# Optimization experiments

Hardware: AMD Instinct MI355X
Metric: run time of the kernel (lower is better)

The kernel has to match this reference:

```python
import jax, jax.numpy as jnp
import numpy as np

VERTS = [5023, 1256, 314, 79, 20]
SPIRAL_LEN = 9
T_FRAMES = 32
LATENT = 64


def _spiral_conv(x, idx, W, b):
    # x: [B, N, C]; idx: [N, L]; gather spiral neighborhoods then linear
    B = x.shape[0]
    g = x[:, idx.reshape(-1), :].reshape(B, idx.shape[0], -1)  # [B, N, L*C]
    return g @ W.T + b


def _pool(x, rows, cols, vals, n_out):
    # sparse matmul: out[b, rows] += x[b, cols] * vals  (index_select + scatter_add)
    gathered = x[:, cols, :] * vals[None, :, None]
    return jnp.zeros((x.shape[0], n_out, x.shape[2]), x.dtype).at[:, rows, :].add(gathered)


def _lstm_dir(x, Wih, Whh, bih, bhh, reverse):
    # x: [T, B, D]; PyTorch gate order i, f, g, o
    Bz, H = x.shape[1], Whh.shape[1]
    bias = bih + bhh
    def step(carry, xt):
        h, c = carry
        g = xt @ Wih.T + h @ Whh.T + bias
        i, f, gg, o = jnp.split(g, 4, axis=-1)
        c = jax.nn.sigmoid(f) * c + jax.nn.sigmoid(i) * jnp.tanh(gg)
        h = jax.nn.sigmoid(o) * jnp.tanh(c)
        return (h, c), h
    init = (jnp.zeros((Bz, H), x.dtype), jnp.zeros((Bz, H), x.dtype))
    _, hs = jax.lax.scan(step, init, x, reverse=reverse)
    return hs


def _forward(audio_hidden, vertices, actor,
             sp_idx0, sp_idx1, sp_idx2, sp_idx3,
             d0_rows, d0_cols, d0_vals, d1_rows, d1_cols, d1_vals,
             d2_rows, d2_cols, d2_vals, d3_rows, d3_cols, d3_vals,
             u0_rows, u0_cols, u0_vals, u1_rows, u1_cols, u1_vals,
             u2_rows, u2_cols, u2_vals, u3_rows, u3_cols, u3_vals,
             enc_W0, enc_b0, enc_W1, enc_b1, enc_W2, enc_b2, enc_W3, enc_b3,
             enc_lin_W, enc_lin_b, dec_lin_W, dec_lin_b,
             dec_W0, dec_b0, dec_W1, dec_b1, dec_W2, dec_b2, dec_W3, dec_b3,
             dec_W4, dec_b4, aud_W, aud_b,
             l0_Wih, l0_Whh, l0_bih, l0_bhh, l12_Wih, l12_Whh, l12_bih, l12_bhh):
    ah = audio_hidden
    if ah.shape[1] % 2 != 0:
        ah = ah[:, :ah.shape[1] - 1]
    tv = vertices.shape[1]
    if ah.shape[1] > 2 * tv:
        ah = ah[:, :2 * tv]
    elif ah.shape[1] < 2 * tv:
        tv = ah.shape[1] // 2
    hs = ah.reshape(1, ah.shape[1] // 2, ah.shape[2] * 2)[:, :tv]  # [1, T, 1536]
    audio_emb = hs @ aud_W.T + aud_b                                # [1, T, LATENT]
    # --- mesh encoder on actor template: (spiral conv -> ELU -> down pool) x4 -> Linear ---
    sp = (sp_idx0, sp_idx1, sp_idx2, sp_idx3)
    down = ((d0_rows, d0_cols, d0_vals), (d1_rows, d1_cols, d1_vals),
            (d2_rows, d2_cols, d2_vals), (d3_rows, d3_cols, d3_vals))
    encp = ((enc_W0, enc_b0), (enc_W1, enc_b1), (enc_W2, enc_b2), (enc_W3, enc_b3))
    x = actor
    for i in range(4):
        x = jax.nn.elu(_spiral_conv(x, sp[i], *encp[i]))
        x = _pool(x, *down[i], VERTS[i + 1])
    z = x.reshape(x.shape[0], -1) @ enc_lin_W.T + enc_lin_b        # [1, LATENT]
    actor_emb = jnp.broadcast_to(z[:, None, :], audio_emb.shape)
    # --- 3-layer bidirectional LSTM ---
    h = jnp.concatenate([audio_emb, actor_emb], axis=-1).transpose(1, 0, 2)  # [T, 1, 2*LATENT]
    for layer in range(3):
        if layer == 0:
            Wih, Whh, bih, bhh = l0_Wih, l0_Whh, l0_bih, l0_bhh
        else:
            Wih, Whh, bih, bhh = l12_Wih[layer - 1], l12_Whh[layer - 1], l12_bih[layer - 1], l12_bhh[layer - 1]
        f = _lstm_dir(h, Wih[0], Whh[0], bih[0], bhh[0], False)
        r = _lstm_dir(h, Wih[1], Whh[1], bih[1], bhh[1], True)
        h = jnp.concatenate([f, r], axis=-1)
    latent = h.transpose(1, 0, 2)[0]                               # [T, LATENT]
    # --- mesh decoder, batched over all frames (replaces the python per-frame loop) ---
    up = ((u0_rows, u0_cols, u0_vals), (u1_rows, u1_cols, u1_vals),
          (u2_rows, u2_cols, u2_vals), (u3_rows, u3_cols, u3_vals))
    decp = ((dec_W0, dec_b0), (dec_W1, dec_b1), (dec_W2, dec_b2), (dec_W3, dec_b3))
    y = latent @ dec_lin_W.T + dec_lin_b                           # [T, 20*256]
    y = y.reshape(y.shape[0], VERTS[4], -1)                        # [T, 20, 256]
    for i in range(4):
        j = 3 - i
        y = _pool(y, *up[j], VERTS[j])
        y = jax.nn.elu(_spiral_conv(y, sp[j], *decp[i]))
    y = _spiral_conv(y, sp[0], dec_W4, dec_b4)                     # [T, 5023, 3]
    return y + actor                                               # broadcast residual, == vstacked preds


def setup_inputs() -> dict:
    key = jax.random.key(0)
    ks = iter(jax.random.split(key, 96))
    def nrm(shape, s=0.05):
        return jax.random.normal(next(ks), shape, jnp.float32) * s
    def rint(shape, hi):
        return jax.random.randint(next(ks), shape, 0, hi)
    inp = {}
    inp['audio_hidden'] = nrm((1, 2 * T_FRAMES, 768), 1.0)
    inp['vertices'] = nrm((1, T_FRAMES, VERTS[0], 3), 1.0)
    inp['actor'] = nrm((1, VERTS[0], 3), 1.0)
    for i in range(4):
        inp['sp_idx%d' % i] = rint((VERTS[i], SPIRAL_LEN), VERTS[i])
    for i in range(4):
        nnz = 3 * VERTS[i + 1]
        inp['d%d_rows' % i] = rint((nnz,), VERTS[i + 1])
        inp['d%d_cols' % i] = rint((nnz,), VERTS[i])
        inp['d%d_vals' % i] = jax.random.uniform(next(ks), (nnz,), jnp.float32)
    for i in range(4):
        nnz = 3 * VERTS[i]
        inp['u%d_rows' % i] = rint((nnz,), VERTS[i])
        inp['u%d_cols' % i] = rint((nnz,), VERTS[i + 1])
        inp['u%d_vals' % i] = jax.random.uniform(next(ks), (nnz,), jnp.float32)
    OC = [32, 64, 128, 256]
    ic = 3
    for i in range(4):
        inp['enc_W%d' % i] = nrm((OC[i], ic * SPIRAL_LEN))
        inp['enc_b%d' % i] = nrm((OC[i],))
        ic = OC[i]
    inp['enc_lin_W'] = nrm((LATENT, VERTS[4] * OC[3]))
    inp['enc_lin_b'] = nrm((LATENT,))
    inp['dec_lin_W'] = nrm((VERTS[4] * OC[3], LATENT))
    inp['dec_lin_b'] = nrm((VERTS[4] * OC[3],))
    dic = [256, 256, 128, 64]
    doc = [256, 128, 64, 32]
    for i in range(4):
        inp['dec_W%d' % i] = nrm((doc[i], dic[i] * SPIRAL_LEN))
        inp['dec_b%d' % i] = nrm((doc[i],))
    inp['dec_W4'] = nrm((3, OC[0] * SPIRAL_LEN))
    inp['dec_b4'] = nrm((3,))
    inp['aud_W'] = nrm((LATENT, 1536))
    inp['aud_b'] = nrm((LATENT,))
    H = LATENT // 2
    inp['l0_Wih'] = nrm((2, 4 * H, 2 * LATENT))
    inp['l0_Whh'] = nrm((2, 4 * H, H))
    inp['l0_bih'] = nrm((2, 4 * H))
    inp['l0_bhh'] = nrm((2, 4 * H))
    inp['l12_Wih'] = nrm((2, 2, 4 * H, 2 * H))
    inp['l12_Whh'] = nrm((2, 2, 4 * H, H))
    inp['l12_bih'] = nrm((2, 2, 4 * H))
    inp['l12_bhh'] = nrm((2, 2, 4 * H))
    return inp


def reference(audio_hidden, vertices, actor,
              sp_idx0, sp_idx1, sp_idx2, sp_idx3,
              d0_rows, d0_cols, d0_vals, d1_rows, d1_cols, d1_vals,
              d2_rows, d2_cols, d2_vals, d3_rows, d3_cols, d3_vals,
              u0_rows, u0_cols, u0_vals, u1_rows, u1_cols, u1_vals,
              u2_rows, u2_cols, u2_vals, u3_rows, u3_cols, u3_vals,
              enc_W0, enc_b0, enc_W1, enc_b1, enc_W2, enc_b2, enc_W3, enc_b3,
              enc_lin_W, enc_lin_b, dec_lin_W, dec_lin_b,
              dec_W0, dec_b0, dec_W1, dec_b1, dec_W2, dec_b2, dec_W3, dec_b3,
              dec_W4, dec_b4, aud_W, aud_b,
              l0_Wih, l0_Whh, l0_bih, l0_bhh, l12_Wih, l12_Whh, l12_bih, l12_bhh):
    return _forward(audio_hidden, vertices, actor,
                    sp_idx0, sp_idx1, sp_idx2, sp_idx3,
                    d0_rows, d0_cols, d0_vals, d1_rows, d1_cols, d1_vals,
                    d2_rows, d2_cols, d2_vals, d3_rows, d3_cols, d3_vals,
                    u0_rows, u0_cols, u0_vals, u1_rows, u1_cols, u1_vals,
                    u2_rows, u2_cols, u2_vals, u3_rows, u3_cols, u3_vals,
                    enc_W0, enc_b0, enc_W1, enc_b1, enc_W2, enc_b2, enc_W3, enc_b3,
                    enc_lin_W, enc_lin_b, dec_lin_W, dec_lin_b,
                    dec_W0, dec_b0, dec_W1, dec_b1, dec_W2, dec_b2, dec_W3, dec_b3,
                    dec_W4, dec_b4, aud_W, aud_b,
                    l0_Wih, l0_Whh, l0_bih, l0_bhh, l12_Wih, l12_Whh, l12_bih, l12_bhh)
```

## Files before the change

kernel.cpp:

```cpp
#include <hip/hip_runtime.h>
#include <cstdint>
#include <cstddef>


typedef unsigned short u16;
typedef __attribute__((ext_vector_type(8))) short short8;
typedef __attribute__((ext_vector_type(4))) float float4v;
#define CDIV(a,b) (((a)+(b)-1)/(b))
#define POOL_CAP 64

__device__ __forceinline__ float bf(u16 u){ return __uint_as_float(((unsigned)u)<<16); }
__device__ __forceinline__ u16 fb(float x){
  unsigned u = __float_as_uint(x);
  unsigned r = u + 0x7fffu + ((u>>16)&1u);
  return (u16)(r>>16);
}
__device__ __forceinline__ float lo16(unsigned u){ return __uint_as_float(u<<16); }
__device__ __forceinline__ float hi16(unsigned u){ return __uint_as_float(u & 0xffff0000u); }

struct WCast { const float* src[7]; int cum[8]; };
__global__ void cast_all_k(WCast C, u16* __restrict__ dst, int total){
  int i = blockIdx.x*blockDim.x + threadIdx.x;
  if (i >= total) return;
  int k = 0;
  while (i >= C.cum[k+1]) k++;
  dst[i] = fb(C.src[k][i - C.cum[k]]);
}

__global__ void audio_emb_k(const float* __restrict__ ah, const float* __restrict__ W,
                            const float* __restrict__ b, float* __restrict__ h0){
  int t = blockIdx.x;
  int f = threadIdx.x >> 2, sl = threadIdx.x & 3;
  const float4* x4 = (const float4*)(ah + t*1536);
  const float4* w4 = (const float4*)(W + f*1536);
  float acc = 0.f;
  for (int k=sl; k<384; k+=4){
    float4 xv = x4[k], wv = w4[k];
    acc += xv.x*wv.x + xv.y*wv.y + xv.z*wv.z + xv.w*wv.w;
  }
  acc += __shfl_down(acc, 2, 64);
  acc += __shfl_down(acc, 1, 64);
  if (sl == 0) h0[t*128 + f] = acc + b[f];
}

__global__ void conv3_k(const float* __restrict__ x, const int* __restrict__ idx,
                        const float* __restrict__ W, const float* __restrict__ bias,
                        u16* __restrict__ out, int V, int OC){
  int i = blockIdx.x*blockDim.x + threadIdx.x;
  if (i >= V*OC) return;
  int o = i % OC; int v = i / OC;
  const float* wrow = W + (size_t)o*27;
  const int* vix = idx + v*9;
  float acc = bias[o];
  for (int s=0;s<9;s++){
    const float* xr = x + (size_t)vix[s]*3;
    acc += xr[0]*wrow[s*3] + xr[1]*wrow[s*3+1] + xr[2]*wrow[s*3+2];
  }
  if (acc < 0.f) acc = expm1f(acc);
  out[i] = fb(acc);
}

template<int IC, int BN, int BM>
__global__ void __launch_bounds__(256) conv_mfma(
    const u16* __restrict__ x, const int* __restrict__ idx,
    const u16* __restrict__ Wb, const float* __restrict__ bias,
    u16* __restrict__ out, int V, int OC, int M){
  constexpr int K = 9*IC;
  constexpr int KC = K/32;
  constexpr int NT = BN/16;
  constexpr int MT = BM/64;
  constexpr int LOG2 = (IC==32?5: IC==64?6: IC==128?7:8);
  constexpr int AST = 40;
  __shared__ u16 Asm[2][BM*AST];
  __shared__ u16 Bsm[2][BN*AST];
  __shared__ int rowB[BM], rowV[BM];
  __shared__ int sidx[BM*9];
  int t = threadIdx.x;
  int m0 = blockIdx.x*BM;
  int o0 = blockIdx.y*BN;
  if (t < BM){
    int mg = m0 + t;
    if (mg < M){ int b = mg / V; rowB[t] = b; rowV[t] = mg - b*V; }
    else rowB[t] = -1;
  }
  __syncthreads();
  for (int i=t; i<BM*9; i+=256){
    int r = i/9, s = i - r*9;
    sidx[i] = (rowB[r] >= 0) ? idx[rowV[r]*9 + s] : 0;
  }
  int lane = t & 63, wave = t >> 6;
  int quad = lane >> 4, col = lane & 15;
  float4v acc[MT][NT];
  #pragma unroll
  for (int mi=0;mi<MT;mi++)
    #pragma unroll
    for (int nt=0;nt<NT;nt++) acc[mi][nt] = (float4v)0.f;

  uint4 aval[MT]; uint4 bval;
  auto fetch = [&](int kc){
    int s  = (kc*32) >> LOG2;
    int c0 = (kc*32) & (IC-1);
    #pragma unroll
    for (int rpt=0; rpt<MT; ++rpt){
      int seg = t + 256*rpt;
      int arow = seg >> 2, aq = seg & 3;
      int b = rowB[arow];
      uint4 v = {0u,0u,0u,0u};
      if (b >= 0){
        int ix = sidx[arow*9 + s];
        v = *(const uint4*)(x + ((size_t)b*V + ix)*IC + c0 + aq*8);
      }
      aval[rpt] = v;
    }
    if (t < BN*4){
      int br = t >> 2, bq = t & 3;
      bval = *(const uint4*)(Wb + (size_t)(o0+br)*K + kc*32 + bq*8);
    }
  };

  __syncthreads();
  fetch(0);

  for (int kc = 0; kc < KC; ++kc){
    int buf = kc & 1;
    #pragma unroll
    for (int rpt=0; rpt<MT; ++rpt){
      int seg = t + 256*rpt;
      int arow = seg >> 2, aq = seg & 3;
      *(uint4*)&Asm[buf][arow*AST + aq*8] = aval[rpt];
    }
    if (t < BN*4){
      int br = t >> 2, bq = t & 3;
      *(uint4*)&Bsm[buf][br*AST + bq*8] = bval;
    }
    __syncthreads();
    if (kc+1 < KC) fetch(kc+1);
    short8 a[MT];
    #pragma unroll
    for (int mi=0;mi<MT;mi++)
      a[mi] = *(const short8*)&Asm[buf][(wave*MT*16 + mi*16 + col)*AST + quad*8];
    #pragma unroll
    for (int nt=0; nt<NT; ++nt){
      short8 bfr = *(const short8*)&Bsm[buf][(nt*16 + col)*AST + quad*8];
      #pragma unroll
      for (int mi=0;mi<MT;mi++)
        acc[mi][nt] = __builtin_amdgcn_mfma_f32_16x16x32_bf16(a[mi], bfr, acc[mi][nt], 0, 0, 0);
    }
  }
  #pragma unroll
  for (int mi=0;mi<MT;mi++){
    #pragma unroll
    for (int nt=0; nt<NT; ++nt){
      int o = o0 + nt*16 + col;
      float bv = bias[o];
      #pragma unroll
      for (int r=0;r<4;r++){
        int mg = m0 + wave*MT*16 + mi*16 + quad*4 + r;
        if (mg < M){
          float val = acc[mi][nt][r] + bv;
          if (val < 0.f) val = expm1f(val);
          out[(size_t)mg*OC + o] = fb(val);
        }
      }
    }
  }
}

struct Lists {
  const int* rows[8];
  int nnz[8];
  int curoff[8];
  int lstoff[8];
};
__global__ void fill_all_k(Lists L, int* __restrict__ curBase, int* __restrict__ lstBase, int total){
  int i = blockIdx.x*blockDim.x + threadIdx.x;
  if (i >= total) return;
  int off = i, k = 0;
  while (off >= L.nnz[k]){ off -= L.nnz[k]; k++; }
  int r = L.rows[k][off];
  int p = atomicAdd(curBase + L.curoff[k] + r, 1);
  if (p < POOL_CAP) lstBase[L.lstoff[k] + r*POOL_CAP + p] = off;
}

__global__ void pool_g4_k(const u16* __restrict__ x, const int* __restrict__ cols,
                          const float* __restrict__ vals, const int* __restrict__ cur,
                          const int* __restrict__ lst, u16* __restrict__ out,
                          int B, int Vin, int Vout, int C){
  int C4 = C >> 2;
  int total = B*Vout*C4;
  int i = blockIdx.x*blockDim.x + threadIdx.x;
  if (i >= total) return;
  int c4 = i % C4; int tt = i / C4; int r = tt % Vout; int b = tt / Vout;
  int deg = cur[r]; if (deg > POOL_CAP) deg = POOL_CAP;
  const int* le = lst + r*POOL_CAP;
  float a0=0.f,a1=0.f,a2=0.f,a3=0.f;
  for (int k=0;k<deg;k++){
    int e = le[k];
    float v = vals[e];
    ushort4 xv = *(const ushort4*)(x + ((size_t)b*Vin + (size_t)cols[e])*C + c4*4);
    a0 += v*bf(xv.x); a1 += v*bf(xv.y); a2 += v*bf(xv.z); a3 += v*bf(xv.w);
  }
  ushort4 o; o.x=fb(a0); o.y=fb(a1); o.z=fb(a2); o.w=fb(a3);
  *(ushort4*)(out + ((size_t)b*Vout + (size_t)r)*C + c4*4) = o;
}

__global__ void __launch_bounds__(256) enc_lin_k(
    const u16* __restrict__ x, const float* __restrict__ W,
    const float* __restrict__ b, float* __restrict__ h0){
  int f = blockIdx.x;
  int t = threadIdx.x;
  const ushort4* x4 = (const ushort4*)x;
  const float4* w4 = (const float4*)(W + (size_t)f*5120);
  float acc = 0.f;
  for (int k=t; k<1280; k+=256){
    ushort4 xv = x4[k]; float4 wv = w4[k];
    acc += bf(xv.x)*wv.x + bf(xv.y)*wv.y + bf(xv.z)*wv.z + bf(xv.w)*wv.w;
  }
  #pragma unroll
  for (int off=32; off; off>>=1) acc += __shfl_down(acc, off, 64);
  __shared__ float red[4];
  if ((t & 63) == 0) red[t>>6] = acc;
  __syncthreads();
  if (t < 32){
    float zf = b[f] + red[0] + red[1] + red[2] + red[3];
    h0[t*128 + 64 + f] = zf;
  }
}

__device__ __forceinline__ float sigm(float x){ return 1.f/(1.f+__expf(-x)); }
__device__ __forceinline__ float tanhfast(float x){ return 1.f - 2.f/(__expf(2.f*x)+1.f); }

__global__ void __launch_bounds__(256) lstm3_k(
    const float* __restrict__ h0,
    const float* __restrict__ l0_Wih, const float* __restrict__ l0_Whh,
    const float* __restrict__ l0_bih, const float* __restrict__ l0_bhh,
    const float* __restrict__ l12_Wih, const float* __restrict__ l12_Whh,
    const float* __restrict__ l12_bih, const float* __restrict__ l12_bhh,
    float* __restrict__ latent){
  __shared__ __align__(16) u16 xb[32*136];
  __shared__ __align__(16) float xp[2*32*128];
  __shared__ __align__(16) u16 obuf[32*64];
  __shared__ __align__(16) u16 hsh[2][32];
  __shared__ float bias_l[256];
  int t = threadIdx.x;
  int lane = t & 63, wave = t >> 6;
  int quad = lane >> 4, col = lane & 15;
  int dir = t >> 7;
  bool rev = (dir == 1);
  int w2 = (t >> 6) & 1;
  int unit = w2*16 + col;
  int jj = quad*32 + unit;

  for (int i=t;i<32*128;i+=256){ int tt=i>>7, k=i&127; xb[tt*136+k]=fb(h0[i]); }

  for (int layer=0; layer<3; layer++){
    int IN = (layer==0)?128:64;
    const float *Wih,*Whh,*bih,*bhh;
    if (layer==0){ Wih=l0_Wih; Whh=l0_Whh; bih=l0_bih; bhh=l0_bhh; }
    else {
      int mb=(layer-1)*2;
      Wih=l12_Wih + (size_t)mb*128*64; Whh=l12_Whh + (size_t)mb*128*32;
      bih=l12_bih + mb*128; bhh=l12_bhh + mb*128;
    }
    const float* WhhD = Whh + (size_t)dir*128*32 + (size_t)jj*32;
    unsigned whh[16];
    #pragma unroll
    for (int k=0;k<16;k++){
      float2 w = *(const float2*)&WhhD[2*k];
      whh[k] = ((unsigned)fb(w.x)) | (((unsigned)fb(w.y))<<16);
    }
    bias_l[t] = bih[dir*128 + (t&127)] + bhh[dir*128 + (t&127)];
    if (quad == 0) hsh[dir][unit] = 0;
    float creg = 0.f;
    __syncthreads();

    {
      int dirA = wave >> 1, o0 = (wave & 1)*64;
      const float* WA = Wih + (size_t)dirA*128*IN;
      float4v acc[2][4];
      #pragma unroll
      for (int mi=0;mi<2;mi++)
        #pragma unroll
        for (int nt=0;nt<4;nt++) acc[mi][nt] = (float4v)0.f;
      for (int kc=0; kc<IN/32; ++kc){
        short8 bfrag[4];
        #pragma unroll
        for (int nt=0;nt<4;nt++){
          const float* src = WA + (size_t)(o0+nt*16+col)*IN + kc*32 + quad*8;
          float4 w0 = *(const float4*)src;
          float4 w1 = *(const float4*)(src+4);
          alignas(16) u16 tmp[8] = {fb(w0.x),fb(w0.y),fb(w0.z),fb(w0.w),
                                    fb(w1.x),fb(w1.y),fb(w1.z),fb(w1.w)};
          bfrag[nt] = *(const short8*)tmp;
        }
        short8 afrag[2];
        #pragma unroll
        for (int mi=0;mi<2;mi++)
          afrag[mi] = *(const short8*)&xb[(mi*16+col)*136 + kc*32 + quad*8];
        #pragma unroll
        for (int nt=0;nt<4;nt++)
          #pragma unroll
          for (int mi=0;mi<2;mi++)
            acc[mi][nt] = __builtin_amdgcn_mfma_f32_16x16x32_bf16(afrag[mi], bfrag[nt], acc[mi][nt], 0, 0, 0);
      }
      #pragma unroll
      for (int mi=0;mi<2;mi++)
        #pragma unroll
        for (int nt=0;nt<4;nt++){
          int j = o0 + nt*16 + col;
          float bv = bias_l[dirA*128 + j];
          #pragma unroll
          for (int r=0;r<4;r++){
            int tt = mi*16 + quad*4 + r;
            xp[dirA*4096 + tt*128 + j] = acc[mi][nt][r] + bv;
          }
        }
    }
    __syncthreads();

    for (int s=0;s<32;s++){
      int tx = rev ? (31-s) : s;
      float g = xp[dir*4096 + tx*128 + jj];
      const uint4* h4 = (const uint4*)hsh[dir];
      float a0=0.f,a1=0.f,a2=0.f,a3=0.f;
      #pragma unroll
      for (int k=0;k<4;k++){
        uint4 hv = h4[k];
        unsigned u0=whh[4*k], u1=whh[4*k+1], u2=whh[4*k+2], u3=whh[4*k+3];
        a0 = fmaf(lo16(hv.x), lo16(u0), a0);
        a0 = fmaf(hi16(hv.x), hi16(u0), a0);
        a1 = fmaf(lo16(hv.y), lo16(u1), a1);
        a1 = fmaf(hi16(hv.y), hi16(u1), a1);
        a2 = fmaf(lo16(hv.z), lo16(u2), a2);
        a2 = fmaf(hi16(hv.z), hi16(u2), a2);
        a3 = fmaf(lo16(hv.w), lo16(u3), a3);
        a3 = fmaf(hi16(hv.w), hi16(u3), a3);
      }
      g += (a0+a1) + (a2+a3);
      float act = (quad == 2) ? tanhfast(g) : sigm(g);
      float gi = __shfl(act, col, 64);
      float gf = __shfl(act, 16+col, 64);
      float gg = __shfl(act, 32+col, 64);
      float go = __shfl(act, 48+col, 64);
      if (quad == 0){
        float cn = gf*creg + gi*gg;
        float hn = go*tanhfast(cn);
        creg = cn;
        u16 hb = fb(hn);
        hsh[dir][unit] = hb;
        obuf[tx*64 + dir*32 + unit] = hb;
      }
      __syncthreads();
    }
    if (layer < 2){
      for (int i=t;i<32*64;i+=256){ int tt=i>>6, k=i&63; xb[tt*136+k]=obuf[i]; }
      __syncthreads();
    }
  }
  for (int i=t;i<32*64;i+=256) latent[i] = bf(obuf[i]);
}

__global__ void dec_lin_k(const float* __restrict__ latent, const float* __restrict__ W,
                          const float* __restrict__ b, u16* __restrict__ y){
  int i = blockIdx.x*blockDim.x + threadIdx.x;
  if (i >= 32*5120) return;
  int r = i % 5120, t = i / 5120;
  const float4* x4 = (const float4*)(latent + t*64);
  const float4* w4 = (const float4*)(W + (size_t)r*64);
  float acc = b[r];
  #pragma unroll
  for (int k=0;k<16;k++){
    float4 xv=x4[k]; float4 wv=w4[k];
    acc += xv.x*wv.x+xv.y*wv.y+xv.z*wv.z+xv.w*wv.w;
  }
  y[i] = fb(acc);
}

__global__ void final_k(const u16* __restrict__ x, const int* __restrict__ idx,
                        const float* __restrict__ W, const float* __restrict__ bias,
                        const float* __restrict__ actor, float* __restrict__ out){
  __shared__ float Wsm[3*288];
  __shared__ float bsm[3];
  int t = threadIdx.x;
  for (int i=t;i<864;i+=256) Wsm[i]=W[i];
  if (t<3) bsm[t]=bias[t];
  __syncthreads();
  int g = blockIdx.x*256 + t;
  if (g >= 32*5023) return;
  int v = g % 5023, b = g / 5023;
  const u16* xb = x + (size_t)b*5023*32;
  const int* vix = idx + v*9;
  float a0=bsm[0], a1=bsm[1], a2=bsm[2];
  for (int s=0;s<9;s++){
    const ushort4* xr = (const ushort4*)(xb + (size_t)vix[s]*32);
    #pragma unroll
    for (int k=0;k<8;k++){
      ushort4 xv = xr[k];
      float x0=bf(xv.x), x1=bf(xv.y), x2=bf(xv.z), x3=bf(xv.w);
      int kk = s*32 + k*4;
      a0 += x0*Wsm[kk] + x1*Wsm[kk+1] + x2*Wsm[kk+2] + x3*Wsm[kk+3];
      a1 += x0*Wsm[288+kk] + x1*Wsm[288+kk+1] + x2*Wsm[288+kk+2] + x3*Wsm[288+kk+3];
      a2 += x0*Wsm[576+kk] + x1*Wsm[576+kk+1] + x2*Wsm[576+kk+2] + x3*Wsm[576+kk+3];
    }
  }
  out[(size_t)g*3+0] = a0 + actor[v*3+0];
  out[(size_t)g*3+1] = a1 + actor[v*3+1];
  out[(size_t)g*3+2] = a2 + actor[v*3+2];
}

extern "C" void kernel_launch(void* const* d_in, const int* in_sizes, int n_in,
                              void* d_out, int out_size, void* d_ws, size_t ws_size,
                              hipStream_t stream){
  (void)in_sizes; (void)n_in; (void)out_size; (void)ws_size;

  const float* audio = (const float*)d_in[0];
  const float* actor = (const float*)d_in[2];
  const int* sp[4]   = {(const int*)d_in[3],(const int*)d_in[4],(const int*)d_in[5],(const int*)d_in[6]};
  const int* drows[4]; const int* dcols[4]; const float* dvals[4];
  for (int i=0;i<4;i++){ drows[i]=(const int*)d_in[7+3*i]; dcols[i]=(const int*)d_in[8+3*i]; dvals[i]=(const float*)d_in[9+3*i]; }
  const int* urows[4]; const int* ucols[4]; const float* uvals[4];
  for (int i=0;i<4;i++){ urows[i]=(const int*)d_in[19+3*i]; ucols[i]=(const int*)d_in[20+3*i]; uvals[i]=(const float*)d_in[21+3*i]; }
  const float* encW[4]={(const float*)d_in[31],(const float*)d_in[33],(const float*)d_in[35],(const float*)d_in[37]};
  const float* encB[4]={(const float*)d_in[32],(const float*)d_in[34],(const float*)d_in[36],(const float*)d_in[38]};
  const float* enc_lin_W=(const float*)d_in[39]; const float* enc_lin_b=(const float*)d_in[40];
  const float* dec_lin_W=(const float*)d_in[41]; const float* dec_lin_b=(const float*)d_in[42];
  const float* decW[5]={(const float*)d_in[43],(const float*)d_in[45],(const float*)d_in[47],(const float*)d_in[49],(const float*)d_in[51]};
  const float* decB[5]={(const float*)d_in[44],(const float*)d_in[46],(const float*)d_in[48],(const float*)d_in[50],(const float*)d_in[52]};
  const float* audW=(const float*)d_in[53]; const float* audB=(const float*)d_in[54];
  const float* l0_Wih=(const float*)d_in[55]; const float* l0_Whh=(const float*)d_in[56];
  const float* l0_bih=(const float*)d_in[57]; const float* l0_bhh=(const float*)d_in[58];
  const float* l12_Wih=(const float*)d_in[59]; const float* l12_Whh=(const float*)d_in[60];
  const float* l12_bih=(const float*)d_in[61]; const float* l12_bhh=(const float*)d_in[62];
  float* out = (float*)d_out;

  char* base = (char*)d_ws;
  u16* A  = (u16*)base;
  u16* Bb = (u16*)(base + 10287104);
  int* curBase = (int*)(base + 30891520);
  int* lstBase = (int*)(base + 30924928);
  u16* Wbf = (u16*)(base + 33060224);
  float* sm = (float*)(base + 35788160);
  float* h0     = sm;
  float* latent = sm + 4096;

  const int wsz[7] = {64*288, 128*576, 256*1152, 256*2304, 128*2304, 64*1152, 32*576};
  WCast WC; int wcum = 0;
  const float* wsrc[7] = {encW[1],encW[2],encW[3],decW[0],decW[1],decW[2],decW[3]};
  int wo[7];
  for (int k=0;k<7;k++){ WC.src[k]=wsrc[k]; WC.cum[k]=wcum; wo[k]=wcum; wcum+=wsz[k]; }
  WC.cum[7]=wcum;
  cast_all_k<<<CDIV(wcum,256),256,0,stream>>>(WC, Wbf, wcum);

  const int pVout[8] = {1256,314,79,20,5023,1256,314,79};
  const int pNnz[8]  = {3768,942,237,60,15069,3768,942,237};
  Lists L; int curoff=0, lstoff=0, totnnz=0;
  const int* prow[8] = {drows[0],drows[1],drows[2],drows[3],urows[0],urows[1],urows[2],urows[3]};
  int curo[8], lsto[8];
  for (int k=0;k<8;k++){
    L.rows[k]=prow[k]; L.nnz[k]=pNnz[k];
    L.curoff[k]=curoff; L.lstoff[k]=lstoff;
    curo[k]=curoff; lsto[k]=lstoff;
    curoff += pVout[k]; lstoff += pVout[k]*POOL_CAP; totnnz += pNnz[k];
  }
  hipMemsetAsync(curBase, 0, (size_t)curoff*4, stream);
  fill_all_k<<<CDIV(totnnz,256),256,0,stream>>>(L, curBase, lstBase, totnnz);

  audio_emb_k<<<32,256,0,stream>>>(audio, audW, audB, h0);

  conv3_k<<<CDIV(5023*32,256),256,0,stream>>>(actor, sp[0], encW[0], encB[0], A, 5023, 32);
  pool_g4_k<<<CDIV(1256*8,256),256,0,stream>>>(A, dcols[0], dvals[0], curBase+curo[0], lstBase+lsto[0], Bb, 1, 5023, 1256, 32);
  conv_mfma<32,64,64><<<dim3(CDIV(1256,64),1),256,0,stream>>>(Bb, sp[1], Wbf+wo[0], encB[1], A, 1256, 64, 1256);
  pool_g4_k<<<CDIV(314*16,256),256,0,stream>>>(A, dcols[1], dvals[1], curBase+curo[1], lstBase+lsto[1], Bb, 1, 1256, 314, 64);
  conv_mfma<64,64,64><<<dim3(CDIV(314,64),2),256,0,stream>>>(Bb, sp[2], Wbf+wo[1], encB[2], A, 314, 128, 314);
  pool_g4_k<<<CDIV(79*32,256),256,0,stream>>>(A, dcols[2], dvals[2], curBase+curo[2], lstBase+lsto[2], Bb, 1, 314, 79, 128);
  conv_mfma<128,64,64><<<dim3(CDIV(79,64),4),256,0,stream>>>(Bb, sp[3], Wbf+wo[2], encB[3], A, 79, 256, 79);
  pool_g4_k<<<CDIV(20*64,256),256,0,stream>>>(A, dcols[3], dvals[3], curBase+curo[3], lstBase+lsto[3], Bb, 1, 79, 20, 256);

  enc_lin_k<<<64,256,0,stream>>>(Bb, enc_lin_W, enc_lin_b, h0);

  lstm3_k<<<1,256,0,stream>>>(h0, l0_Wih, l0_Whh, l0_bih, l0_bhh,
                              l12_Wih, l12_Whh, l12_bih, l12_bhh, latent);

  dec_lin_k<<<CDIV(32*5120,256),256,0,stream>>>(latent, dec_lin_W, dec_lin_b, A);

  pool_g4_k<<<CDIV(32*79*64,256),256,0,stream>>>(A, ucols[3], uvals[3], curBase+curo[7], lstBase+lsto[7], Bb, 32, 20, 79, 256);
  conv_mfma<256,64,64><<<dim3(CDIV(2528,64),4),256,0,stream>>>(Bb, sp[3], Wbf+wo[3], decB[0], A, 79, 256, 2528);

  pool_g4_k<<<CDIV(32*314*64,256),256,0,stream>>>(A, ucols[2], uvals[2], curBase+curo[6], lstBase+lsto[6], Bb, 32, 79, 314, 256);
  conv_mfma<256,64,64><<<dim3(CDIV(10048,64),2),256,0,stream>>>(Bb, sp[2], Wbf+wo[4], decB[1], A, 314, 128, 10048);

  pool_g4_k<<<CDIV(32*1256*32,256),256,0,stream>>>(A, ucols[1], uvals[1], curBase+curo[5], lstBase+lsto[5], Bb, 32, 314, 1256, 128);
  conv_mfma<128,64,128><<<dim3(CDIV(40192,128),1),256,0,stream>>>(Bb, sp[1], Wbf+wo[5], decB[2], A, 1256, 64, 40192);

  pool_g4_k<<<CDIV(32*5023*16,256),256,0,stream>>>(A, ucols[0], uvals[0], curBase+curo[4], lstBase+lsto[4], Bb, 32, 1256, 5023, 64);
  conv_mfma<64,32,128><<<dim3(CDIV(160736,128),1),256,0,stream>>>(Bb, sp[0], Wbf+wo[6], decB[3], A, 5023, 32, 160736);

  final_k<<<CDIV(32*5023,256),256,0,stream>>>(A, sp[0], decW[4], decB[4], actor, out);
}
```

Measured before the change: 591.0 us.

## Fuse setup kernels into one launch and run LSTM recurrence on single waves

Four independent setup kernels (pool list fill, weight cast, audio embedding, first spiral conv) are merged into one launch that dispatches on block index, cutting launch overhead. The LSTM recurrence now runs one wave per direction, with each lane holding two gate rows of Whh in registers and broadcasting the hidden state through wave shuffles. This removes the block-wide __syncthreads on every timestep. In exchange only two of four waves work during the recurrence, and each lane does twice the FMAs plus 32 shuffles per step.

```diff
diff --git a/kernel.cpp b/kernel.cpp
--- a/kernel.cpp
+++ b/kernel.cpp
@@ -19,45 +19,73 @@
 __device__ __forceinline__ float hi16(unsigned u){ return __uint_as_float(u & 0xffff0000u); }
 
 struct WCast { const float* src[7]; int cum[8]; };
-__global__ void cast_all_k(WCast C, u16* __restrict__ dst, int total){
-  int i = blockIdx.x*blockDim.x + threadIdx.x;
-  if (i >= total) return;
-  int k = 0;
-  while (i >= C.cum[k+1]) k++;
-  dst[i] = fb(C.src[k][i - C.cum[k]]);
-}
-
-__global__ void audio_emb_k(const float* __restrict__ ah, const float* __restrict__ W,
-                            const float* __restrict__ b, float* __restrict__ h0){
-  int t = blockIdx.x;
-  int f = threadIdx.x >> 2, sl = threadIdx.x & 3;
-  const float4* x4 = (const float4*)(ah + t*1536);
-  const float4* w4 = (const float4*)(W + f*1536);
-  float acc = 0.f;
-  for (int k=sl; k<384; k+=4){
-    float4 xv = x4[k], wv = w4[k];
-    acc += xv.x*wv.x + xv.y*wv.y + xv.z*wv.z + xv.w*wv.w;
-  }
-  acc += __shfl_down(acc, 2, 64);
-  acc += __shfl_down(acc, 1, 64);
-  if (sl == 0) h0[t*128 + f] = acc + b[f];
-}
-
-__global__ void conv3_k(const float* __restrict__ x, const int* __restrict__ idx,
-                        const float* __restrict__ W, const float* __restrict__ bias,
-                        u16* __restrict__ out, int V, int OC){
-  int i = blockIdx.x*blockDim.x + threadIdx.x;
-  if (i >= V*OC) return;
-  int o = i % OC; int v = i / OC;
-  const float* wrow = W + (size_t)o*27;
-  const int* vix = idx + v*9;
-  float acc = bias[o];
+struct Lists {
+  const int* rows[8];
+  int nnz[8];
+  int curoff[8];
+  int lstoff[8];
+};
+
+__global__ void __launch_bounds__(256) setup_k(
+    Lists L, int totN, int NF, int* __restrict__ curBase, int* __restrict__ lstBase,
+    WCast C, int totW, int NC, u16* __restrict__ Wbf,
+    const float* __restrict__ audio, const float* __restrict__ audW,
+    const float* __restrict__ audB, float* __restrict__ h0,
+    const float* __restrict__ actor, const int* __restrict__ sp0,
+    const float* __restrict__ encW0, const float* __restrict__ encB0,
+    u16* __restrict__ outA){
+  int blk = blockIdx.x;
+  int tid = threadIdx.x;
+  if (blk < NF){
+    int i = blk*256 + tid;
+    if (i < totN){
+      int off = i, k = 0;
+      while (off >= L.nnz[k]){ off -= L.nnz[k]; k++; }
+      int r = L.rows[k][off];
+      int p = atomicAdd(curBase + L.curoff[k] + r, 1);
+      if (p < POOL_CAP) lstBase[L.lstoff[k] + r*POOL_CAP + p] = off;
+    }
+    return;
+  }
+  blk -= NF;
+  if (blk < NC){
+    int i = blk*256 + tid;
+    if (i < totW){
+      int k = 0;
+      while (i >= C.cum[k+1]) k++;
+      Wbf[i] = fb(C.src[k][i - C.cum[k]]);
+    }
+    return;
+  }
+  blk -= NC;
+  if (blk < 32){
+    int t = blk;
+    int f = tid >> 2, sl = tid & 3;
+    const float4* x4 = (const float4*)(audio + t*1536);
+    const float4* w4 = (const float4*)(audW + f*1536);
+    float acc = 0.f;
+    for (int k=sl; k<384; k+=4){
+      float4 xv = x4[k], wv = w4[k];
+      acc += xv.x*wv.x + xv.y*wv.y + xv.z*wv.z + xv.w*wv.w;
+    }
+    acc += __shfl_down(acc, 2, 64);
+    acc += __shfl_down(acc, 1, 64);
+    if (sl == 0) h0[t*128 + f] = acc + audB[f];
+    return;
+  }
+  blk -= 32;
+  int i = blk*256 + tid;
+  if (i >= 5023*32) return;
+  int o = i % 32; int v = i / 32;
+  const float* wrow = encW0 + (size_t)o*27;
+  const int* vix = sp0 + v*9;
+  float acc = encB0[o];
   for (int s=0;s<9;s++){
-    const float* xr = x + (size_t)vix[s]*3;
+    const float* xr = actor + (size_t)vix[s]*3;
     acc += xr[0]*wrow[s*3] + xr[1]*wrow[s*3+1] + xr[2]*wrow[s*3+2];
   }
   if (acc < 0.f) acc = expm1f(acc);
-  out[i] = fb(acc);
+  outA[i] = fb(acc);
 }
 
 template<int IC, int BN, int BM>
@@ -166,22 +194,6 @@
   }
 }
 
-struct Lists {
-  const int* rows[8];
-  int nnz[8];
-  int curoff[8];
-  int lstoff[8];
-};
-__global__ void fill_all_k(Lists L, int* __restrict__ curBase, int* __restrict__ lstBase, int total){
-  int i = blockIdx.x*blockDim.x + threadIdx.x;
-  if (i >= total) return;
-  int off = i, k = 0;
-  while (off >= L.nnz[k]){ off -= L.nnz[k]; k++; }
-  int r = L.rows[k][off];
-  int p = atomicAdd(curBase + L.curoff[k] + r, 1);
-  if (p < POOL_CAP) lstBase[L.lstoff[k] + r*POOL_CAP + p] = off;
-}
-
 __global__ void pool_g4_k(const u16* __restrict__ x, const int* __restrict__ cols,
                           const float* __restrict__ vals, const int* __restrict__ cur,
                           const int* __restrict__ lst, u16* __restrict__ out,
@@ -240,16 +252,10 @@
   __shared__ __align__(16) u16 xb[32*136];
   __shared__ __align__(16) float xp[2*32*128];
   __shared__ __align__(16) u16 obuf[32*64];
-  __shared__ __align__(16) u16 hsh[2][32];
   __shared__ float bias_l[256];
   int t = threadIdx.x;
   int lane = t & 63, wave = t >> 6;
   int quad = lane >> 4, col = lane & 15;
-  int dir = t >> 7;
-  bool rev = (dir == 1);
-  int w2 = (t >> 6) & 1;
-  int unit = w2*16 + col;
-  int jj = quad*32 + unit;
 
   for (int i=t;i<32*128;i+=256){ int tt=i>>7, k=i&127; xb[tt*136+k]=fb(h0[i]); }
 
@@ -262,16 +268,7 @@
       Wih=l12_Wih + (size_t)mb*128*64; Whh=l12_Whh + (size_t)mb*128*32;
       bih=l12_bih + mb*128; bhh=l12_bhh + mb*128;
     }
-    const float* WhhD = Whh + (size_t)dir*128*32 + (size_t)jj*32;
-    unsigned whh[16];
-    #pragma unroll
-    for (int k=0;k<16;k++){
-      float2 w = *(const float2*)&WhhD[2*k];
-      whh[k] = ((unsigned)fb(w.x)) | (((unsigned)fb(w.y))<<16);
-    }
-    bias_l[t] = bih[dir*128 + (t&127)] + bhh[dir*128 + (t&127)];
-    if (quad == 0) hsh[dir][unit] = 0;
-    float creg = 0.f;
+    bias_l[t] = bih[(t>>7)*128 + (t&127)] + bhh[(t>>7)*128 + (t&127)];
     __syncthreads();
 
     {
@@ -318,40 +315,56 @@
     }
     __syncthreads();
 
-    for (int s=0;s<32;s++){
-      int tx = rev ? (31-s) : s;
-      float g = xp[dir*4096 + tx*128 + jj];
-      const uint4* h4 = (const uint4*)hsh[dir];
-      float a0=0.f,a1=0.f,a2=0.f,a3=0.f;
+    if (wave < 2){
+      int dir = wave;
+      bool rev = (dir == 1);
+      int u = lane & 31, gp = lane >> 5;
+      int jj0 = gp*64 + u;
+      int jj1 = gp*64 + 32 + u;
+      const float* W0 = Whh + (size_t)dir*128*32 + (size_t)jj0*32;
+      const float* W1 = Whh + (size_t)dir*128*32 + (size_t)jj1*32;
+      unsigned wa[16], wb[16];
       #pragma unroll
-      for (int k=0;k<4;k++){
-        uint4 hv = h4[k];
-        unsigned u0=whh[4*k], u1=whh[4*k+1], u2=whh[4*k+2], u3=whh[4*k+3];
-        a0 = fmaf(lo16(hv.x), lo16(u0), a0);
-        a0 = fmaf(hi16(hv.x), hi16(u0), a0);
-        a1 = fmaf(lo16(hv.y), lo16(u1), a1);
-        a1 = fmaf(hi16(hv.y), hi16(u1), a1);
-        a2 = fmaf(lo16(hv.z), lo16(u2), a2);
-        a2 = fmaf(hi16(hv.z), hi16(u2), a2);
-        a3 = fmaf(lo16(hv.w), lo16(u3), a3);
-        a3 = fmaf(hi16(hv.w), hi16(u3), a3);
+      for (int k=0;k<16;k++){
+        float2 w0 = *(const float2*)&W0[2*k];
+        float2 w1 = *(const float2*)&W1[2*k];
+        wa[k] = ((unsigned)fb(w0.x)) | (((unsigned)fb(w0.y))<<16);
+        wb[k] = ((unsigned)fb(w1.x)) | (((unsigned)fb(w1.y))<<16);
       }
-      g += (a0+a1) + (a2+a3);
-      float act = (quad == 2) ? tanhfast(g) : sigm(g);
-      float gi = __shfl(act, col, 64);
-      float gf = __shfl(act, 16+col, 64);
-      float gg = __shfl(act, 32+col, 64);
-      float go = __shfl(act, 48+col, 64);
-      if (quad == 0){
-        float cn = gf*creg + gi*gg;
+      float h[32];
+      #pragma unroll
+      for (int k=0;k<32;k++) h[k] = 0.f;
+      float creg = 0.f;
+      const float* xpd = xp + dir*4096;
+
+      for (int s=0;s<32;s++){
+        int tx = rev ? (31-s) : s;
+        float g0 = xpd[tx*128 + jj0];
+        float g1 = xpd[tx*128 + jj1];
+        float p0=0.f,q0=0.f,p1=0.f,q1=0.f;
+        #pragma unroll
+        for (int k=0;k<16;k++){
+          unsigned ua = wa[k], ub = wb[k];
+          p0 = fmaf(h[2*k],   lo16(ua), p0);
+          q0 = fmaf(h[2*k+1], hi16(ua), q0);
+          p1 = fmaf(h[2*k],   lo16(ub), p1);
+          q1 = fmaf(h[2*k+1], hi16(ub), q1);
+        }
+        g0 += p0 + q0;
+        g1 += p1 + q1;
+        float act0 = (gp == 1) ? tanhfast(g0) : sigm(g0);
+        float act1 = sigm(g1);
+        float gg = __shfl(act0, 32 + u, 64);
+        float go = __shfl(act1, 32 + u, 64);
+        float cn = act1*creg + act0*gg;
         float hn = go*tanhfast(cn);
-        creg = cn;
-        u16 hb = fb(hn);
-        hsh[dir][unit] = hb;
-        obuf[tx*64 + dir*32 + unit] = hb;
+        creg = (gp == 0) ? cn : 0.f;
+        #pragma unroll
+        for (int k=0;k<32;k++) h[k] = __shfl(hn, k, 64);
+        if (gp == 0) obuf[tx*64 + dir*32 + u] = fb(hn);
       }
-      __syncthreads();
-    }
+    }
+    __syncthreads();
     if (layer < 2){
       for (int i=t;i<32*64;i+=256){ int tt=i>>6, k=i&63; xb[tt*136+k]=obuf[i]; }
       __syncthreads();
@@ -449,7 +462,6 @@
   int wo[7];
   for (int k=0;k<7;k++){ WC.src[k]=wsrc[k]; WC.cum[k]=wcum; wo[k]=wcum; wcum+=wsz[k]; }
   WC.cum[7]=wcum;
-  cast_all_k<<<CDIV(wcum,256),256,0,stream>>>(WC, Wbf, wcum);
 
   const int pVout[8] = {1256,314,79,20,5023,1256,314,79};
   const int pNnz[8]  = {3768,942,237,60,15069,3768,942,237};
@@ -463,11 +475,13 @@
     curoff += pVout[k]; lstoff += pVout[k]*POOL_CAP; totnnz += pNnz[k];
   }
   hipMemsetAsync(curBase, 0, (size_t)curoff*4, stream);
-  fill_all_k<<<CDIV(totnnz,256),256,0,stream>>>(L, curBase, lstBase, totnnz);
-
-  audio_emb_k<<<32,256,0,stream>>>(audio, audW, audB, h0);
-
-  conv3_k<<<CDIV(5023*32,256),256,0,stream>>>(actor, sp[0], encW[0], encB[0], A, 5023, 32);
+
+  int NF = CDIV(totnnz,256), NC = CDIV(wcum,256), NC3 = CDIV(5023*32,256);
+  setup_k<<<NF+NC+32+NC3,256,0,stream>>>(L, totnnz, NF, curBase, lstBase,
+                                         WC, wcum, NC, Wbf,
+                                         audio, audW, audB, h0,
+                                         actor, sp[0], encW[0], encB[0], A);
+
   pool_g4_k<<<CDIV(1256*8,256),256,0,stream>>>(A, dcols[0], dvals[0], curBase+curo[0], lstBase+lsto[0], Bb, 1, 5023, 1256, 32);
   conv_mfma<32,64,64><<<dim3(CDIV(1256,64),1),256,0,stream>>>(Bb, sp[1], Wbf+wo[0], encB[1], A, 1256, 64, 1256);
   pool_g4_k<<<CDIV(314*16,256),256,0,stream>>>(A, dcols[1], dvals[1], curBase+curo[1], lstBase+lsto[1], Bb, 1, 1256, 314, 64);
```

Measured after the change: 593.7 us. Within noise of the previous version (+0.5%).
